# Performance work log

Hardware: AMD Instinct MI355X
Metric: run time of the kernel (lower is better)

Reference implementation:

```python
import jax, jax.numpy as jnp
import numpy as np
from jax import lax

B, C, W, H, K = 4, 32, 256, 256, 9
CENTER = K // 2
EXTEND = 1.0
EPS = 1e-5


def conv2d(x, w, b, stride=(1, 1), padding='SAME'):
    y = lax.conv_general_dilated(x, w, stride, padding,
                                 dimension_numbers=('NCHW', 'OIHW', 'NCHW'))
    return y + b[None, :, None, None]


def group_norm(x, scale, bias, groups):
    b, c, h, w = x.shape
    xg = x.reshape(b, groups, c // groups, h, w)
    mu = xg.mean(axis=(2, 3, 4), keepdims=True)
    var = xg.var(axis=(2, 3, 4), keepdims=True)
    xn = ((xg - mu) * lax.rsqrt(var + EPS)).reshape(b, c, h, w)
    return xn * scale[None, :, None, None] + bias[None, :, None, None]


def bilinear_sample(feat, py, px):
    # feat: (C, W, H); py, px: (W*K, H) pixel coords, already clamped in-range
    y0 = jnp.floor(py)
    x0 = jnp.floor(px)
    wy = py - y0
    wx = px - x0
    y0i = jnp.clip(y0, 0, W - 1).astype(jnp.int32)
    y1i = jnp.clip(y0 + 1, 0, W - 1).astype(jnp.int32)
    x0i = jnp.clip(x0, 0, H - 1).astype(jnp.int32)
    x1i = jnp.clip(x0 + 1, 0, H - 1).astype(jnp.int32)
    v00 = feat[:, y0i, x0i]
    v01 = feat[:, y0i, x1i]
    v10 = feat[:, y1i, x0i]
    v11 = feat[:, y1i, x1i]
    return (v00 * (1 - wy) * (1 - wx) + v01 * (1 - wy) * wx
            + v10 * wy * (1 - wx) + v11 * wy * wx)


def ds_conv(x, w_off, b_off, gn_off_scale, gn_off_bias, w_dsc, b_dsc, gn_scale, gn_bias):
    # offset branch: conv3x3 -> GroupNorm(K groups, 2K ch) -> tanh
    off = jnp.tanh(group_norm(conv2d(x, w_off, b_off), gn_off_scale, gn_off_bias, K))
    y_off = off[:, :K]  # (B, K, W, H); x-half of offsets unused when morph == 0
    # cumulative offset scan outward from center tap (center tap offset is 0)
    low = jnp.flip(jnp.cumsum(jnp.flip(y_off[:, :CENTER], 1), 1), 1)
    up = jnp.cumsum(y_off[:, CENTER + 1:], 1)
    y_cum = jnp.concatenate([low, jnp.zeros_like(y_off[:, :1]), up], axis=1)
    # coordinate maps (morph == 0: kernel spreads along x, offsets bend y)
    y_new = jnp.arange(W, dtype=x.dtype)[None, None, :, None] + y_cum * EXTEND
    x_new = (jnp.arange(H, dtype=x.dtype)[None, None, None, :]
             + jnp.linspace(-CENTER, CENTER, K, dtype=x.dtype)[None, :, None, None])
    x_new = jnp.broadcast_to(x_new, y_new.shape)
    gy = y_new.transpose(0, 2, 1, 3).reshape(-1, W * K, H)  # 'b k w h -> b (w k) h'
    gx = x_new.transpose(0, 2, 1, 3).reshape(-1, W * K, H)
    # normalize as torch grid_sample (align_corners=True) with clamp to [-1, 1]
    gy = jnp.clip(gy / W * 2 - 1, -1.0, 1.0)
    gx = jnp.clip(gx / H * 2 - 1, -1.0, 1.0)
    py = (gy + 1) * 0.5 * (W - 1)
    px = (gx + 1) * 0.5 * (H - 1)
    deformed = jax.vmap(bilinear_sample)(x, py, px)  # (B, C, W*K, H)
    out = conv2d(deformed, w_dsc, b_dsc, stride=(K, 1), padding='VALID')  # (B, C, W, H)
    out = group_norm(out, gn_scale, gn_bias, C // 4)
    return jax.nn.relu(out)


def setup_inputs() -> dict:
    key = jax.random.key(0)
    ks = jax.random.split(key, 3)
    return {
        'input': jax.random.normal(ks[0], (B, C, W, H), jnp.float32),
        'w_off': jax.random.normal(ks[1], (2 * K, C, 3, 3), jnp.float32) * 0.05,
        'b_off': jnp.zeros((2 * K,), jnp.float32),
        'gn_off_scale': jnp.ones((2 * K,), jnp.float32),
        'gn_off_bias': jnp.zeros((2 * K,), jnp.float32),
        'w_dsc': jax.random.normal(ks[2], (C, C, K, 1), jnp.float32) * 0.05,
        'b_dsc': jnp.zeros((C,), jnp.float32),
        'gn_scale': jnp.ones((C,), jnp.float32),
        'gn_bias': jnp.zeros((C,), jnp.float32),
    }


def reference(input, w_off, b_off, gn_off_scale, gn_off_bias, w_dsc, b_dsc, gn_scale, gn_bias):
    # in_channels == out_channels so input_adjust is Identity
    return ds_conv(input, w_off, b_off, gn_off_scale, gn_off_bias, w_dsc, b_dsc, gn_scale, gn_bias)
```

## Files before the change

kernel.cpp:

```cpp
#include <hip/hip_runtime.h>
#include <hip/hip_bf16.h>

#define BB 4
#define CC 32
#define WW 256
#define HH 256
#define WH (WW*HH)

typedef __attribute__((ext_vector_type(8))) short bf16x8;
typedef __attribute__((ext_vector_type(4))) short bf16x4;
typedef __attribute__((ext_vector_type(4))) float f32x4;

__device__ __forceinline__ short f2bf(float x) {
    union { float f; unsigned u; } a; a.f = x;
    unsigned r = (a.u + 0x7FFF + ((a.u >> 16) & 1)) >> 16;
    return (short)r;
}

__global__ void k0_init(const float* __restrict__ w_dsc, const float* __restrict__ w_off,
                        unsigned short* __restrict__ B3f, unsigned short* __restrict__ B8f,
                        unsigned short* __restrict__ B1f, unsigned short* __restrict__ B18f,
                        float* __restrict__ stats1, float* __restrict__ stats2) {
    int i = blockIdx.x * 256 + threadIdx.x;
    if (i < 8192) {
        int j = i & 7, l = (i >> 3) & 63, nt = (i >> 9) & 1, ch = i >> 10;
        int o = nt * 16 + (l & 15);
        int kl = ((l >> 4) << 3) | j;
        int tap = kl >> 2, cl = kl & 3;
        B3f[i] = (unsigned short)f2bf(w_dsc[(o * 32 + ch * 4 + cl) * 9 + tap]);
    } else if (i < 9216) {
        int e = i - 8192;
        int j = e & 7, l = (e >> 3) & 63, nt = e >> 9;
        int o = nt * 16 + (l & 15);
        int k8 = ((l >> 4) << 3) | j;
        B8f[e] = (unsigned short)f2bf(w_dsc[(o * 32 + k8) * 9 + 8]);
    } else if (i < 13312) {
        int e = i - 9216;
        int j = e & 7, l = (e >> 3) & 63, ch = e >> 9;
        int o = l & 15;
        int kl = ((l >> 4) << 3) | j;
        int tap = kl >> 2, cl = kl & 3;
        B1f[e] = (o < 10) ? (unsigned short)f2bf(w_off[(o * 32 + ch * 4 + cl) * 9 + tap]) : 0;
    } else if (i < 13824) {
        int e = i - 13312;
        int j = e & 7, l = (e >> 3) & 63;
        int o = l & 15;
        int k8 = ((l >> 4) << 3) | j;
        B18f[e] = (o < 10) ? (unsigned short)f2bf(w_off[(o * 32 + k8) * 9 + 8]) : 0;
    }
    if (i < 40) stats1[i] = 0.f;
    if (i < 64) stats2[i] = 0.f;
}

__global__ __launch_bounds__(256, 3) void k1_conv(
    const float* __restrict__ x, const unsigned short* __restrict__ B1f,
    const unsigned short* __restrict__ B18f, const float* __restrict__ b_off,
    float* __restrict__ off_buf, float* __restrict__ stats1) {
    __shared__ __align__(16) unsigned short tbf[4 * 132 * 4];
    __shared__ float scr[40];
    __shared__ __align__(16) short Apan[16 * 64 * 8];
    __shared__ __align__(16) short A8pan[16 * 64 * 8];

    const int b = blockIdx.z;
    const int w0 = blockIdx.y * 2;
    const int h0 = blockIdx.x * 128;
    const int p = threadIdx.x;
    const int lane = p & 63;
    const int wv = p >> 6;
    const int hl = p & 127;
    const int wi = p >> 7;
    const int mt = p >> 4;
    const int mrow = p & 15;

    bf16x8 Bf[8], B8g;
    {
        const bf16x8* bp = (const bf16x8*)B1f;
#pragma unroll
        for (int ch = 0; ch < 8; ++ch) Bf[ch] = bp[ch * 64 + lane];
        B8g = ((const bf16x8*)B18f)[lane];
    }

    f32x4 acc[4];
#pragma unroll
    for (int i = 0; i < 4; ++i) acc[i] = (f32x4){0.f, 0.f, 0.f, 0.f};

    const float* xb = x + (size_t)b * CC * WH;

    int tio1[9], go1[9];
#pragma unroll
    for (int u = 0; u < 9; ++u) {
        int t = p + u * 256;
        if (t < 2080) {
            int c = t / 520;
            int rem = t - c * 520;
            int r = rem / 130;
            int cl = rem - r * 130;
            int y = w0 - 1 + r;
            int g = h0 - 1 + cl;
            tio1[u] = (r * 132 + cl) * 4 + c;
            go1[u] = (y >= 0 && y < 256 && g >= 0 && g < 256)
                     ? (c * WH + y * 256 + g) : -1;
        } else { tio1[u] = -1; go1[u] = -1; }
    }

#pragma unroll
    for (int ch = 0; ch < 8; ++ch) {
        const int cb = ch * 4 * WH;
#pragma unroll
        for (int u = 0; u < 9; ++u) {
            if (tio1[u] >= 0) {
                unsigned short v = 0;
                if (go1[u] >= 0) v = (unsigned short)f2bf(xb[cb + go1[u]]);
                tbf[tio1[u]] = v;
            }
        }
        __syncthreads();

#pragma unroll
        for (int kg = 0; kg < 4; ++kg) {
            bf16x4 lo, hi;
            {
                int tap = kg * 2, dy = tap / 3, dx = tap - dy * 3;
                lo = *(const bf16x4*)&tbf[((wi + dy) * 132 + hl + dx) * 4];
            }
            {
                int tap = kg * 2 + 1, dy = tap / 3, dx = tap - dy * 3;
                hi = *(const bf16x4*)&tbf[((wi + dy) * 132 + hl + dx) * 4];
            }
            bf16x8 pv;
#pragma unroll
            for (int e = 0; e < 4; ++e) { pv[e] = lo[e]; pv[4 + e] = hi[e]; }
            *(bf16x8*)&Apan[mt * 512 + (kg * 16 + mrow) * 8] = pv;
        }
        {
            bf16x4 pv8 = *(const bf16x4*)&tbf[((wi + 2) * 132 + hl + 2) * 4];
            *(bf16x4*)&A8pan[mt * 512 + ((ch >> 1) * 16 + mrow) * 8 + (ch & 1) * 4] = pv8;
        }
        __syncthreads();

#pragma unroll
        for (int i = 0; i < 4; ++i) {
            bf16x8 a = *(const bf16x8*)&Apan[((wv * 4 + i) * 64 + lane) * 8];
            acc[i] = __builtin_amdgcn_mfma_f32_16x16x32_bf16(a, Bf[ch], acc[i], 0, 0, 0);
        }
    }
#pragma unroll
    for (int i = 0; i < 4; ++i) {
        bf16x8 a = *(const bf16x8*)&A8pan[((wv * 4 + i) * 64 + lane) * 8];
        acc[i] = __builtin_amdgcn_mfma_f32_16x16x32_bf16(a, B8g, acc[i], 0, 0, 0);
    }

    const int oc = lane & 15;
    float bias = (oc < 10) ? b_off[oc] : 0.f;
#pragma unroll
    for (int i = 0; i < 4; ++i)
#pragma unroll
        for (int r = 0; r < 4; ++r) acc[i][r] += bias;

    if (oc < 10) {
#pragma unroll
        for (int i = 0; i < 4; ++i) {
            int px = (wv * 4 + i) * 16 + (lane >> 4) * 4;
            size_t addr = (size_t)(b * 10 + oc) * WH +
                          (size_t)(w0 + (px >> 7)) * 256 + h0 + (px & 127);
            *(f32x4*)&off_buf[addr] = acc[i];
        }
    }

    float s = 0.f, q = 0.f;
#pragma unroll
    for (int i = 0; i < 4; ++i)
#pragma unroll
        for (int r = 0; r < 4; ++r) { float v = acc[i][r]; s += v; q += v * v; }
    s += __shfl_xor(s, 1, 64);  q += __shfl_xor(q, 1, 64);
    s += __shfl_xor(s, 16, 64); q += __shfl_xor(q, 16, 64);
    s += __shfl_xor(s, 32, 64); q += __shfl_xor(q, 32, 64);
    __syncthreads();
    if (lane < 10 && !(lane & 1)) {
        int g = lane >> 1;
        scr[(g * 2 + 0) * 4 + wv] = s;
        scr[(g * 2 + 1) * 4 + wv] = q;
    }
    __syncthreads();
    if (threadIdx.x < 10) {
        int g = threadIdx.x >> 1, which = threadIdx.x & 1;
        float sum = scr[(g * 2 + which) * 4 + 0] + scr[(g * 2 + which) * 4 + 1] +
                    scr[(g * 2 + which) * 4 + 2] + scr[(g * 2 + which) * 4 + 3];
        atomicAdd(&stats1[(b * 5 + g) * 2 + which], sum);
    }
}

__global__ __launch_bounds__(256, 2) void k3_sample(
    const float* __restrict__ xin, const float* __restrict__ off_buf,
    const float* __restrict__ stats1, const float* __restrict__ go_scale,
    const float* __restrict__ go_bias, const unsigned short* __restrict__ B3f,
    const unsigned short* __restrict__ B8f, const float* __restrict__ b_dsc,
    float* __restrict__ pre_out, float* __restrict__ stats2) {
    __shared__ float tile[4 * 14 * 96];
    __shared__ short Apan[16 * 64 * 8];
    __shared__ short A8pan[16 * 64 * 8];

    const int b = blockIdx.z;
    const int w0 = blockIdx.y * 4;
    const int h0 = blockIdx.x * 64;
    const int p = threadIdx.x;
    const int lane = p & 63;
    const int wv = p >> 6;
    const int h = h0 + (p & 63);
    const int w = w0 + (p >> 6);
    const int mt = p >> 4;
    const int mrow = p & 15;
    const int row0 = w0 - 5;
    const int col0 = h0 - 8;

    bf16x8 Bf[8][2], B8g[2];
    {
        const bf16x8* bp = (const bf16x8*)B3f;
#pragma unroll
        for (int ch = 0; ch < 8; ++ch) {
            Bf[ch][0] = bp[(ch * 2 + 0) * 64 + lane];
            Bf[ch][1] = bp[(ch * 2 + 1) * 64 + lane];
        }
        B8g[0] = ((const bf16x8*)B8f)[lane];
        B8g[1] = ((const bf16x8*)B8f)[64 + lane];
    }

    const float INV1 = 1.f / (2.f * WH);
    float t9[9];
    size_t obase = (size_t)b * 10 * WH + (size_t)w * 256 + h;
#pragma unroll
    for (int c = 0; c < 9; ++c) {
        float v = off_buf[obase + (size_t)c * WH];
        int g = c >> 1;
        float s1 = stats1[(b * 5 + g) * 2 + 0];
        float q1 = stats1[(b * 5 + g) * 2 + 1];
        float mean = s1 * INV1;
        float istd = rsqrtf(fmaf(q1, INV1, -(mean * mean)) + 1e-5f);
        v = (v - mean) * istd * go_scale[c] + go_bias[c];
        t9[c] = tanhf(v);
    }
    float ycum[9];
    ycum[3] = t9[3];
    ycum[2] = ycum[3] + t9[2];
    ycum[1] = ycum[2] + t9[1];
    ycum[0] = ycum[1] + t9[0];
    ycum[4] = 0.f;
    ycum[5] = t9[5];
    ycum[6] = ycum[5] + t9[6];
    ycum[7] = ycum[6] + t9[7];
    ycum[8] = ycum[7] + t9[8];

    f32x4 acc[4][2];
#pragma unroll
    for (int i = 0; i < 4; ++i) {
        acc[i][0] = (f32x4){0.f, 0.f, 0.f, 0.f};
        acc[i][1] = (f32x4){0.f, 0.f, 0.f, 0.f};
    }

    const float* xb = xin + (size_t)b * CC * WH;
    const float SC = 255.f / 256.f;

#pragma unroll
    for (int ch = 0; ch < 8; ++ch) {
        for (int t = threadIdx.x; t < 1064; t += 256) {
            int c = t / 266;
            int rem = t - c * 266;
            int r = rem / 19;
            int cf = rem - r * 19;
            int y = min(max(row0 + r, 0), 255);
            int g0 = col0 + (cf << 2);
            const float* src = xb + (size_t)(ch * 4 + c) * WH + y * 256;
            float4 val;
            if (g0 >= 0 && g0 <= 252) {
                val = *(const float4*)(src + g0);
            } else {
                val.x = src[min(max(g0, 0), 255)];
                val.y = src[min(max(g0 + 1, 0), 255)];
                val.z = src[min(max(g0 + 2, 0), 255)];
                val.w = src[min(max(g0 + 3, 0), 255)];
            }
            *(float4*)(tile + (c * 14 + r) * 96 + (cf << 2)) = val;
        }
        __syncthreads();

#pragma unroll
        for (int kg = 0; kg < 4; ++kg) {
            bf16x8 pv;
#pragma unroll
            for (int t = 0; t < 2; ++t) {
                int k = kg * 2 + t;
                float py = fminf(fmaxf(((float)w + ycum[k]) * SC, 0.f), 255.f);
                float pxc = fminf(fmaxf((float)(h + k - 4) * SC, 0.f), 255.f);
                float y0f = floorf(py), x0f = floorf(pxc);
                float wy = py - y0f, wx = pxc - x0f;
                int r0 = (int)y0f - row0;
                int r1 = min((int)y0f + 1, 255) - row0;
                int tc = (int)x0f - col0;
                float w00 = (1.f - wy) * (1.f - wx);
                float w01 = (1.f - wy) * wx;
                float w10 = wy * (1.f - wx);
                float w11 = wy * wx;
#pragma unroll
                for (int cl = 0; cl < 4; ++cl) {
                    const float* p0 = tile + (cl * 14 + r0) * 96 + tc;
                    const float* p1 = tile + (cl * 14 + r1) * 96 + tc;
                    float v = fmaf(w00, p0[0],
                              fmaf(w01, p0[1], fmaf(w10, p1[0], w11 * p1[1])));
                    pv[t * 4 + cl] = f2bf(v);
                }
            }
            *(bf16x8*)&Apan[mt * 512 + (kg * 16 + mrow) * 8] = pv;
        }
        {
            float py = fminf(fmaxf(((float)w + ycum[8]) * SC, 0.f), 255.f);
            float pxc = fminf(fmaxf((float)(h + 4) * SC, 0.f), 255.f);
            float y0f = floorf(py), x0f = floorf(pxc);
            float wy = py - y0f, wx = pxc - x0f;
            int r0 = (int)y0f - row0;
            int r1 = min((int)y0f + 1, 255) - row0;
            int tc = (int)x0f - col0;
            float w00 = (1.f - wy) * (1.f - wx);
            float w01 = (1.f - wy) * wx;
            float w10 = wy * (1.f - wx);
            float w11 = wy * wx;
            bf16x4 pv8;
#pragma unroll
            for (int cl = 0; cl < 4; ++cl) {
                const float* p0 = tile + (cl * 14 + r0) * 96 + tc;
                const float* p1 = tile + (cl * 14 + r1) * 96 + tc;
                float v = fmaf(w00, p0[0],
                          fmaf(w01, p0[1], fmaf(w10, p1[0], w11 * p1[1])));
                pv8[cl] = f2bf(v);
            }
            *(bf16x4*)&A8pan[mt * 512 + ((ch >> 1) * 16 + mrow) * 8 + (ch & 1) * 4] = pv8;
        }
        __syncthreads();

#pragma unroll
        for (int i = 0; i < 4; ++i) {
            bf16x8 a = *(const bf16x8*)&Apan[((wv * 4 + i) * 64 + lane) * 8];
            acc[i][0] = __builtin_amdgcn_mfma_f32_16x16x32_bf16(a, Bf[ch][0], acc[i][0], 0, 0, 0);
            acc[i][1] = __builtin_amdgcn_mfma_f32_16x16x32_bf16(a, Bf[ch][1], acc[i][1], 0, 0, 0);
        }
    }
#pragma unroll
    for (int i = 0; i < 4; ++i) {
        bf16x8 a = *(const bf16x8*)&A8pan[((wv * 4 + i) * 64 + lane) * 8];
        acc[i][0] = __builtin_amdgcn_mfma_f32_16x16x32_bf16(a, B8g[0], acc[i][0], 0, 0, 0);
        acc[i][1] = __builtin_amdgcn_mfma_f32_16x16x32_bf16(a, B8g[1], acc[i][1], 0, 0, 0);
    }

    const int oc0 = lane & 15;
    float bias0 = b_dsc[oc0];
    float bias1 = b_dsc[16 + oc0];
#pragma unroll
    for (int i = 0; i < 4; ++i)
#pragma unroll
        for (int r = 0; r < 4; ++r) { acc[i][0][r] += bias0; acc[i][1][r] += bias1; }

#pragma unroll
    for (int i = 0; i < 4; ++i) {
        int px = (wv * 4 + i) * 16 + (lane >> 4) * 4;
        size_t rowoff = (size_t)(w0 + (px >> 6)) * 256 + h0 + (px & 63);
        *(f32x4*)&pre_out[(size_t)(b * 32 + oc0) * WH + rowoff] = acc[i][0];
        *(f32x4*)&pre_out[(size_t)(b * 32 + 16 + oc0) * WH + rowoff] = acc[i][1];
    }

    float s0 = 0.f, q0 = 0.f, s1 = 0.f, q1 = 0.f;
#pragma unroll
    for (int i = 0; i < 4; ++i)
#pragma unroll
        for (int r = 0; r < 4; ++r) {
            float v0 = acc[i][0][r], v1 = acc[i][1][r];
            s0 += v0; q0 += v0 * v0; s1 += v1; q1 += v1 * v1;
        }
#pragma unroll
    for (int m = 0; m < 4; ++m) {
        int d = (m == 0) ? 1 : (m == 1) ? 2 : (m == 2) ? 16 : 32;
        s0 += __shfl_xor(s0, d, 64); q0 += __shfl_xor(q0, d, 64);
        s1 += __shfl_xor(s1, d, 64); q1 += __shfl_xor(q1, d, 64);
    }
    __syncthreads();
    float* scratch = tile;
    if (lane < 16 && !(lane & 3)) {
        int g = lane >> 2;
        scratch[((0 * 4 + g) * 2 + 0) * 4 + wv] = s0;
        scratch[((0 * 4 + g) * 2 + 1) * 4 + wv] = q0;
        scratch[((1 * 4 + g) * 2 + 0) * 4 + wv] = s1;
        scratch[((1 * 4 + g) * 2 + 1) * 4 + wv] = q1;
    }
    __syncthreads();
    if (threadIdx.x < 16) {
        int gg = threadIdx.x >> 1, which = threadIdx.x & 1;
        float sum = scratch[(gg * 2 + which) * 4 + 0] + scratch[(gg * 2 + which) * 4 + 1] +
                    scratch[(gg * 2 + which) * 4 + 2] + scratch[(gg * 2 + which) * 4 + 3];
        atomicAdd(&stats2[(b * 8 + gg) * 2 + which], sum);
    }
}

__global__ __launch_bounds__(256) void k5_gn(float4* __restrict__ out,
                                             const float* __restrict__ stats2,
                                             const float* __restrict__ gs,
                                             const float* __restrict__ gb) {
    int idx = blockIdx.x * 256 + threadIdx.x;
    int bo = idx >> 14;
    int b = bo >> 5;
    int o = bo & 31;
    int g = o >> 2;
    const float INV2 = 1.f / (4.f * WH);
    float s = stats2[(b * 8 + g) * 2 + 0];
    float q = stats2[(b * 8 + g) * 2 + 1];
    float mean = s * INV2;
    float istd = rsqrtf(fmaf(q, INV2, -(mean * mean)) + 1e-5f);
    float sc = gs[o] * istd;
    float bi = gb[o] - mean * sc;
    float4 v = out[idx];
    v.x = fmaxf(fmaf(v.x, sc, bi), 0.f);
    v.y = fmaxf(fmaf(v.y, sc, bi), 0.f);
    v.z = fmaxf(fmaf(v.z, sc, bi), 0.f);
    v.w = fmaxf(fmaf(v.w, sc, bi), 0.f);
    out[idx] = v;
}

extern "C" void kernel_launch(void* const* d_in, const int* in_sizes, int n_in,
                              void* d_out, int out_size, void* d_ws, size_t ws_size,
                              hipStream_t stream) {
    const float* x        = (const float*)d_in[0];
    const float* w_off    = (const float*)d_in[1];
    const float* b_off    = (const float*)d_in[2];
    const float* go_scale = (const float*)d_in[3];
    const float* go_bias  = (const float*)d_in[4];
    const float* w_dsc    = (const float*)d_in[5];
    const float* b_dsc    = (const float*)d_in[6];
    const float* gn_scale = (const float*)d_in[7];
    const float* gn_bias  = (const float*)d_in[8];
    float* out = (float*)d_out;

    float* ws = (float*)d_ws;
    float* off_buf = ws;
    unsigned short* B3f  = (unsigned short*)(ws + 2621440);
    unsigned short* B8f  = (unsigned short*)(ws + 2625536);
    unsigned short* B1f  = (unsigned short*)(ws + 2626048);
    unsigned short* B18f = (unsigned short*)(ws + 2628096);
    float* stats1 = ws + 2628352;
    float* stats2 = stats1 + 80;

    k0_init<<<54, 256, 0, stream>>>(w_dsc, w_off, B3f, B8f, B1f, B18f, stats1, stats2);
    k1_conv<<<dim3(2, 128, BB), 256, 0, stream>>>(x, B1f, B18f, b_off, off_buf, stats1);
    k3_sample<<<dim3(4, 64, BB), 256, 0, stream>>>(x, off_buf, stats1, go_scale, go_bias,
                                                   B3f, B8f, b_dsc, out, stats2);
    k5_gn<<<8192, 256, 0, stream>>>((float4*)out, stats2, gn_scale, gn_bias);
}
```

Before: 216.2 us.

## Stage full conv input tile in LDS upfront with float4 loads

```diff
diff --git a/kernel.cpp b/kernel.cpp
--- a/kernel.cpp
+++ b/kernel.cpp
@@ -52,11 +52,11 @@
     if (i < 64) stats2[i] = 0.f;
 }
 
-__global__ __launch_bounds__(256, 3) void k1_conv(
+__global__ __launch_bounds__(256, 2) void k1_conv(
     const float* __restrict__ x, const unsigned short* __restrict__ B1f,
     const unsigned short* __restrict__ B18f, const float* __restrict__ b_off,
     float* __restrict__ off_buf, float* __restrict__ stats1) {
-    __shared__ __align__(16) unsigned short tbf[4 * 132 * 4];
+    __shared__ __align__(16) unsigned short tbf[8 * 4 * 4 * 136];
     __shared__ float scr[40];
     __shared__ __align__(16) short Apan[16 * 64 * 8];
     __shared__ __align__(16) short A8pan[16 * 64 * 8];
@@ -72,6 +72,28 @@
     const int mt = p >> 4;
     const int mrow = p & 15;
 
+    const float* xb = x + (size_t)b * CC * WH;
+
+#pragma unroll
+    for (int u = 0; u < 17; ++u) {
+        int t = p + u * 256;
+        int g = t / 544;
+        int rem = t - g * 544;
+        int c = rem / 136;
+        int rem2 = rem - c * 136;
+        int r = rem2 / 34;
+        int k = rem2 - r * 34;
+        int y = w0 - 1 + r;
+        int g0 = h0 - 4 + (k << 2);
+        float4 val = {0.f, 0.f, 0.f, 0.f};
+        if (y >= 0 && y < 256 && g0 >= 0 && g0 <= 252)
+            val = *(const float4*)(xb + (size_t)(g * 4 + c) * WH + y * 256 + g0);
+        bf16x4 pv;
+        pv[0] = f2bf(val.x); pv[1] = f2bf(val.y);
+        pv[2] = f2bf(val.z); pv[3] = f2bf(val.w);
+        *(bf16x4*)&tbf[((g * 4 + r) * 4 + c) * 136 + (k << 2)] = pv;
+    }
+
     bf16x8 Bf[8], B8g;
     {
         const bf16x8* bp = (const bf16x8*)B1f;
@@ -84,56 +106,29 @@
 #pragma unroll
     for (int i = 0; i < 4; ++i) acc[i] = (f32x4){0.f, 0.f, 0.f, 0.f};
 
-    const float* xb = x + (size_t)b * CC * WH;
-
-    int tio1[9], go1[9];
-#pragma unroll
-    for (int u = 0; u < 9; ++u) {
-        int t = p + u * 256;
-        if (t < 2080) {
-            int c = t / 520;
-            int rem = t - c * 520;
-            int r = rem / 130;
-            int cl = rem - r * 130;
-            int y = w0 - 1 + r;
-            int g = h0 - 1 + cl;
-            tio1[u] = (r * 132 + cl) * 4 + c;
-            go1[u] = (y >= 0 && y < 256 && g >= 0 && g < 256)
-                     ? (c * WH + y * 256 + g) : -1;
-        } else { tio1[u] = -1; go1[u] = -1; }
-    }
+    __syncthreads();
 
 #pragma unroll
     for (int ch = 0; ch < 8; ++ch) {
-        const int cb = ch * 4 * WH;
-#pragma unroll
-        for (int u = 0; u < 9; ++u) {
-            if (tio1[u] >= 0) {
-                unsigned short v = 0;
-                if (go1[u] >= 0) v = (unsigned short)f2bf(xb[cb + go1[u]]);
-                tbf[tio1[u]] = v;
+#pragma unroll
+        for (int kg = 0; kg < 4; ++kg) {
+            bf16x8 pv;
+#pragma unroll
+            for (int t = 0; t < 2; ++t) {
+                int tap = kg * 2 + t;
+                int dy = tap / 3, dx = tap - dy * 3;
+                int base = ((ch * 4 + wi + dy) * 4) * 136 + (hl + dx + 3);
+#pragma unroll
+                for (int c = 0; c < 4; ++c)
+                    pv[t * 4 + c] = (short)tbf[base + c * 136];
             }
-        }
-        __syncthreads();
-
-#pragma unroll
-        for (int kg = 0; kg < 4; ++kg) {
-            bf16x4 lo, hi;
-            {
-                int tap = kg * 2, dy = tap / 3, dx = tap - dy * 3;
-                lo = *(const bf16x4*)&tbf[((wi + dy) * 132 + hl + dx) * 4];
-            }
-            {
-                int tap = kg * 2 + 1, dy = tap / 3, dx = tap - dy * 3;
-                hi = *(const bf16x4*)&tbf[((wi + dy) * 132 + hl + dx) * 4];
-            }
-            bf16x8 pv;
-#pragma unroll
-            for (int e = 0; e < 4; ++e) { pv[e] = lo[e]; pv[4 + e] = hi[e]; }
             *(bf16x8*)&Apan[mt * 512 + (kg * 16 + mrow) * 8] = pv;
         }
         {
-            bf16x4 pv8 = *(const bf16x4*)&tbf[((wi + 2) * 132 + hl + 2) * 4];
+            int base = ((ch * 4 + wi + 2) * 4) * 136 + (hl + 5);
+            bf16x4 pv8;
+#pragma unroll
+            for (int c = 0; c < 4; ++c) pv8[c] = (short)tbf[base + c * 136];
             *(bf16x4*)&A8pan[mt * 512 + ((ch >> 1) * 16 + mrow) * 8 + (ch & 1) * 4] = pv8;
         }
         __syncthreads();
@@ -143,6 +138,7 @@
             bf16x8 a = *(const bf16x8*)&Apan[((wv * 4 + i) * 64 + lane) * 8];
             acc[i] = __builtin_amdgcn_mfma_f32_16x16x32_bf16(a, Bf[ch], acc[i], 0, 0, 0);
         }
+        __syncthreads();
     }
 #pragma unroll
     for (int i = 0; i < 4; ++i) {
```

New measurement: 211.8 us. 1.02x faster.

## Prefetch full input tile for offset conv with vectorized float4 loads

Applied to the files above, without the earlier changes.

```diff
diff --git a/kernel.cpp b/kernel.cpp
--- a/kernel.cpp
+++ b/kernel.cpp
@@ -52,11 +52,11 @@
     if (i < 64) stats2[i] = 0.f;
 }
 
-__global__ __launch_bounds__(256, 3) void k1_conv(
+__global__ __launch_bounds__(256, 2) void k1_conv(
     const float* __restrict__ x, const unsigned short* __restrict__ B1f,
     const unsigned short* __restrict__ B18f, const float* __restrict__ b_off,
     float* __restrict__ off_buf, float* __restrict__ stats1) {
-    __shared__ __align__(16) unsigned short tbf[4 * 132 * 4];
+    __shared__ __align__(16) unsigned short tbf[8 * 4 * 136 * 4];
     __shared__ float scr[40];
     __shared__ __align__(16) short Apan[16 * 64 * 8];
     __shared__ __align__(16) short A8pan[16 * 64 * 8];
@@ -72,6 +72,37 @@
     const int mt = p >> 4;
     const int mrow = p & 15;
 
+    const float* xb = x + (size_t)b * CC * WH;
+
+#pragma unroll
+    for (int u = 0; u < 5; ++u) {
+        if (u < 4 || p < 64) {
+            int s = p + u * 256;
+            int g = s / 136;
+            int rem = s - g * 136;
+            int r = rem / 34;
+            int k = rem - r * 34;
+            int y = w0 - 1 + r;
+            int g0 = h0 - 4 + (k << 2);
+            f32x4 v0 = {0.f,0.f,0.f,0.f}, v1 = v0, v2 = v0, v3 = v0;
+            if (y >= 0 && y < 256 && g0 >= 0 && g0 <= 252) {
+                const float* bp2 = xb + y * 256 + g0;
+                v0 = *(const f32x4*)(bp2 + (size_t)(g * 4 + 0) * WH);
+                v1 = *(const f32x4*)(bp2 + (size_t)(g * 4 + 1) * WH);
+                v2 = *(const f32x4*)(bp2 + (size_t)(g * 4 + 2) * WH);
+                v3 = *(const f32x4*)(bp2 + (size_t)(g * 4 + 3) * WH);
+            }
+            int base = ((g * 4 + r) * 136 + (k << 2)) * 4;
+#pragma unroll
+            for (int i = 0; i < 4; ++i) {
+                bf16x4 pv;
+                pv[0] = f2bf(v0[i]); pv[1] = f2bf(v1[i]);
+                pv[2] = f2bf(v2[i]); pv[3] = f2bf(v3[i]);
+                *(bf16x4*)&tbf[base + i * 4] = pv;
+            }
+        }
+    }
+
     bf16x8 Bf[8], B8g;
     {
         const bf16x8* bp = (const bf16x8*)B1f;
@@ -84,48 +115,20 @@
 #pragma unroll
     for (int i = 0; i < 4; ++i) acc[i] = (f32x4){0.f, 0.f, 0.f, 0.f};
 
-    const float* xb = x + (size_t)b * CC * WH;
-
-    int tio1[9], go1[9];
-#pragma unroll
-    for (int u = 0; u < 9; ++u) {
-        int t = p + u * 256;
-        if (t < 2080) {
-            int c = t / 520;
-            int rem = t - c * 520;
-            int r = rem / 130;
-            int cl = rem - r * 130;
-            int y = w0 - 1 + r;
-            int g = h0 - 1 + cl;
-            tio1[u] = (r * 132 + cl) * 4 + c;
-            go1[u] = (y >= 0 && y < 256 && g >= 0 && g < 256)
-                     ? (c * WH + y * 256 + g) : -1;
-        } else { tio1[u] = -1; go1[u] = -1; }
-    }
+    __syncthreads();
 
 #pragma unroll
     for (int ch = 0; ch < 8; ++ch) {
-        const int cb = ch * 4 * WH;
-#pragma unroll
-        for (int u = 0; u < 9; ++u) {
-            if (tio1[u] >= 0) {
-                unsigned short v = 0;
-                if (go1[u] >= 0) v = (unsigned short)f2bf(xb[cb + go1[u]]);
-                tbf[tio1[u]] = v;
-            }
-        }
-        __syncthreads();
-
 #pragma unroll
         for (int kg = 0; kg < 4; ++kg) {
             bf16x4 lo, hi;
             {
                 int tap = kg * 2, dy = tap / 3, dx = tap - dy * 3;
-                lo = *(const bf16x4*)&tbf[((wi + dy) * 132 + hl + dx) * 4];
+                lo = *(const bf16x4*)&tbf[((ch * 4 + wi + dy) * 136 + hl + dx + 3) * 4];
             }
             {
                 int tap = kg * 2 + 1, dy = tap / 3, dx = tap - dy * 3;
-                hi = *(const bf16x4*)&tbf[((wi + dy) * 132 + hl + dx) * 4];
+                hi = *(const bf16x4*)&tbf[((ch * 4 + wi + dy) * 136 + hl + dx + 3) * 4];
             }
             bf16x8 pv;
 #pragma unroll
@@ -133,7 +136,7 @@
             *(bf16x8*)&Apan[mt * 512 + (kg * 16 + mrow) * 8] = pv;
         }
         {
-            bf16x4 pv8 = *(const bf16x4*)&tbf[((wi + 2) * 132 + hl + 2) * 4];
+            bf16x4 pv8 = *(const bf16x4*)&tbf[((ch * 4 + wi + 2) * 136 + hl + 5) * 4];
             *(bf16x4*)&A8pan[mt * 512 + ((ch >> 1) * 16 + mrow) * 8 + (ch & 1) * 4] = pv8;
         }
         __syncthreads();
@@ -143,6 +146,7 @@
             bf16x8 a = *(const bf16x8*)&Apan[((wv * 4 + i) * 64 + lane) * 8];
             acc[i] = __builtin_amdgcn_mfma_f32_16x16x32_bf16(a, Bf[ch], acc[i], 0, 0, 0);
         }
+        __syncthreads();
     }
 #pragma unroll
     for (int i = 0; i < 4; ++i) {
```

New measurement: 206.2 us. 4.6% less time.
